# Performance work log

Measured on AMD Instinct MI355X. Metric: run time of the kernel, lower is better.

## Reference

```python
import jax, jax.numpy as jnp
import numpy as np

B, N, K = 16, 1024, 20
IN_DIM, OUT_DIM = 3, 40
LIN_DIM, HID = 1024, 512
EPS = 1e-5
NEG = 0.2  # leaky relu slope (act_kwargs negative_slope=0.2)


def setup_inputs() -> dict:
    key = jax.random.key(0)
    ks = jax.random.split(key, 9)
    def w(k, shp, scale=0.05):
        return jax.random.normal(k, shp, jnp.float32) * scale
    return {
        "pos": jax.random.normal(ks[0], (B, N, IN_DIM), jnp.float32),
        "k": K,
        "W1": w(ks[1], (2 * IN_DIM, 64)), "b1": jnp.zeros((64,), jnp.float32),
        "W2": w(ks[2], (128, 64)),        "b2": jnp.zeros((64,), jnp.float32),
        "W3": w(ks[3], (128, 128)),       "b3": jnp.zeros((128,), jnp.float32),
        "W4": w(ks[4], (256, 256)),       "b4": jnp.zeros((256,), jnp.float32),
        "Wl": w(ks[5], (512, LIN_DIM)),   "bl": jnp.zeros((LIN_DIM,), jnp.float32),
        "gl": jnp.ones((LIN_DIM,), jnp.float32), "betal": jnp.zeros((LIN_DIM,), jnp.float32),
        "Wm1": w(ks[6], (LIN_DIM, HID)),  "bm1": jnp.zeros((HID,), jnp.float32),
        "gm1": jnp.ones((HID,), jnp.float32), "betam1": jnp.zeros((HID,), jnp.float32),
        "Wm2": w(ks[7], (HID, OUT_DIM)),  "bm2": jnp.zeros((OUT_DIM,), jnp.float32),
    }


def _bn(x, g, b):
    # training-mode batch norm over axis 0 (biased variance, eps=1e-5)
    m = jnp.mean(x, axis=0)
    v = jnp.var(x, axis=0)
    return g * (x - m) * jax.lax.rsqrt(v + EPS) + b


def _leaky(x):
    return jnp.where(x > 0, x, NEG * x)


def _edge_conv(x, W, b, k):
    # x: [B,N,d]. Dynamic kNN on current features, edge feat [x_i, x_j - x_i],
    # single Linear (PyG MLP plain_last), max over k neighbors (self included).
    def per_cloud(xc):  # [N,d]
        n, d = xc.shape
        sq = jnp.sum(xc * xc, axis=1)
        dist = sq[:, None] + sq[None, :] - 2.0 * (xc @ xc.T)  # [N,N]
        _, idx = jax.lax.top_k(-dist, k)                       # [N,k] nearest (incl self)
        xj = xc[idx]                                           # [N,k,d]
        xi = xc[:, None, :]
        e = jnp.concatenate([jnp.broadcast_to(xi, (n, k, d)), xj - xi], axis=-1)
        h = e @ W + b                                          # [N,k,out]
        return jnp.max(h, axis=1)                              # [N,out]
    return jax.vmap(per_cloud)(x)


def reference(pos, k, W1, b1, W2, b2, W3, b3, W4, b4,
              Wl, bl, gl, betal, Wm1, bm1, gm1, betam1, Wm2, bm2):
    x1 = _edge_conv(pos, W1, b1, k)   # [B,N,64]
    x2 = _edge_conv(x1, W2, b2, k)    # [B,N,64]
    x3 = _edge_conv(x2, W3, b3, k)    # [B,N,128]
    x4 = _edge_conv(x3, W4, b4, k)    # [B,N,256]
    cat = jnp.concatenate([x1, x2, x3, x4], axis=-1)  # [B,N,512]
    Bn, Nn, C = cat.shape
    flat = cat.reshape(Bn * Nn, C)
    lin = _leaky(_bn(flat @ Wl + bl, gl, betal))      # [B*N,1024]
    pooled = jnp.max(lin.reshape(Bn, Nn, -1), axis=1) # global max pool -> [B,1024]
    h = _leaky(_bn(pooled @ Wm1 + bm1, gm1, betam1))  # [B,512] (dropout omitted)
    return h @ Wm2 + bm2                              # [B,40]
```

## Files before the change

kernel.cpp:

```cpp
#include <hip/hip_runtime.h>
#include <float.h>

#define NB 16
#define NP 1024
#define NROW (NB*NP)

__global__ void k_init(float* colsum, float* colsq, float* pmax, float* pmin) {
    int i = blockIdx.x * 256 + threadIdx.x;
    if (i < 1024) { colsum[i] = 0.f; colsq[i] = 0.f; }
    pmax[i] = -FLT_MAX;
    pmin[i] =  FLT_MAX;
}

__global__ void k_prep(const float* __restrict__ W, const float* __restrict__ b,
                       float* __restrict__ wc, float* __restrict__ b2, int d, int dout) {
    int n2 = 2 * dout;
    int i = blockIdx.x * 256 + threadIdx.x;
    if (i < d * n2) {
        int kk = i / n2, c = i % n2;
        wc[i] = (c < dout) ? (W[kk * dout + c] - W[(kk + d) * dout + c])
                           : W[(kk + d) * dout + (c - dout)];
    }
    if (i < n2) b2[i] = (i < dout) ? b[i] : 0.f;
}

__global__ void k_sqnorm(const float* __restrict__ x, int stride, int D, float* __restrict__ sq) {
    int row = blockIdx.x * 4 + (threadIdx.x >> 6);
    int lane = threadIdx.x & 63;
    const float* xr = x + (size_t)row * stride;
    float s = 0.f;
    for (int kk = lane; kk < D; kk += 64) { float v = xr[kk]; s += v * v; }
    for (int o = 32; o; o >>= 1) s += __shfl_down(s, o);
    if (lane == 0) sq[row] = s;
}

__device__ inline unsigned ford(float f) {
    unsigned u = __float_as_uint(f);
    return (u & 0x80000000u) ? ~u : (u | 0x80000000u);
}

#define FMA16(a, bv) do { \
    acc[0].x += (a).x*(bv).x; acc[0].y += (a).x*(bv).y; acc[0].z += (a).x*(bv).z; acc[0].w += (a).x*(bv).w; \
    acc[1].x += (a).y*(bv).x; acc[1].y += (a).y*(bv).y; acc[1].z += (a).y*(bv).z; acc[1].w += (a).y*(bv).w; \
    acc[2].x += (a).z*(bv).x; acc[2].y += (a).z*(bv).y; acc[2].z += (a).z*(bv).z; acc[2].w += (a).z*(bv).w; \
    acc[3].x += (a).w*(bv).x; acc[3].y += (a).w*(bv).y; acc[3].z += (a).w*(bv).z; acc[3].w += (a).w*(bv).w; \
} while (0)

template<int D>
__global__ __launch_bounds__(256) void k_dist(const float* __restrict__ x, int stride,
                                              const float* __restrict__ sq,
                                              float* __restrict__ dist, int pass) {
    constexpr int KC = (D > 64) ? 64 : D;
    __shared__ __align__(16) float At[KC * 68];
    __shared__ __align__(16) float Bt[KC * 64];
    const int tid = threadIdx.x;
    const int tx = tid & 15, ty = tid >> 4;
    const int j0 = blockIdx.x * 64;
    const int r0 = blockIdx.y * 64;
    const int c8 = blockIdx.z;
    const int bb = pass * 8 + c8;

    float4 acc[4] = {};
    for (int k0 = 0; k0 < D; k0 += KC) {
        __syncthreads();
        if constexpr (KC % 4 == 0) {
            constexpr int K4 = KC / 4;
            for (int e = tid; e < 64 * K4; e += 256) {
                int rr = e / K4, kq = e % K4;
                float4 v = *(const float4*)(x + (size_t)(bb * NP + r0 + rr) * stride + k0 + kq * 4);
                At[(4 * kq + 0) * 68 + rr] = v.x;
                At[(4 * kq + 1) * 68 + rr] = v.y;
                At[(4 * kq + 2) * 68 + rr] = v.z;
                At[(4 * kq + 3) * 68 + rr] = v.w;
            }
            for (int e = tid; e < 64 * K4; e += 256) {
                int jj = e / K4, kq = e % K4;
                float4 v = *(const float4*)(x + (size_t)(bb * NP + j0 + jj) * stride + k0 + kq * 4);
                Bt[(4 * kq + 0) * 64 + jj] = v.x;
                Bt[(4 * kq + 1) * 64 + jj] = v.y;
                Bt[(4 * kq + 2) * 64 + jj] = v.z;
                Bt[(4 * kq + 3) * 64 + jj] = v.w;
            }
        } else {
            for (int e = tid; e < 64 * KC; e += 256) {
                int rr = e / KC, kk = e % KC;
                At[kk * 68 + rr] = x[(size_t)(bb * NP + r0 + rr) * stride + k0 + kk];
            }
            for (int e = tid; e < 64 * KC; e += 256) {
                int jj = e / KC, kk = e % KC;
                Bt[kk * 64 + jj] = x[(size_t)(bb * NP + j0 + jj) * stride + k0 + kk];
            }
        }
        __syncthreads();
#pragma unroll 8
        for (int kk = 0; kk < KC; kk++) {
            float4 a = *(const float4*)&At[kk * 68 + ty * 4];
            float4 bv = *(const float4*)&Bt[kk * 64 + tx * 4];
            FMA16(a, bv);
        }
    }
    float4 sqv = *(const float4*)(sq + bb * NP + j0 + tx * 4);
#pragma unroll
    for (int ri = 0; ri < 4; ri++) {
        float4 o;
        o.x = sqv.x - 2.f * acc[ri].x;
        o.y = sqv.y - 2.f * acc[ri].y;
        o.z = sqv.z - 2.f * acc[ri].z;
        o.w = sqv.w - 2.f * acc[ri].w;
        *(float4*)(dist + (size_t)(c8 * NP + r0 + ty * 4 + ri) * NP + j0 + tx * 4) = o;
    }
}

__global__ __launch_bounds__(256) void k_select(const float* __restrict__ dist,
                                                int* __restrict__ idxout, int pass) {
    const int w = threadIdx.x >> 6, lane = threadIdx.x & 63;
    const int rowlocal = blockIdx.x * 4 + w;
    const size_t base = (size_t)rowlocal * NP;
    const int growrow = pass * 8 * NP + rowlocal;

    unsigned long long pk[16];
    const float4* dp = (const float4*)(dist + base + lane * 16);
#pragma unroll
    for (int q = 0; q < 4; q++) {
        float4 v = dp[q];
        int jb = lane * 16 + q * 4;
        pk[q * 4 + 0] = ((unsigned long long)ford(v.x) << 32) | (unsigned)(jb + 0);
        pk[q * 4 + 1] = ((unsigned long long)ford(v.y) << 32) | (unsigned)(jb + 1);
        pk[q * 4 + 2] = ((unsigned long long)ford(v.z) << 32) | (unsigned)(jb + 2);
        pk[q * 4 + 3] = ((unsigned long long)ford(v.w) << 32) | (unsigned)(jb + 3);
    }
    unsigned msk = 0;
#pragma unroll 1
    for (int it = 0; it < 20; it++) {
        unsigned long long m = 0xFFFFFFFFFFFFFFFFULL;
#pragma unroll
        for (int t = 0; t < 16; t++) {
            unsigned long long v = (msk & (1u << t)) ? 0xFFFFFFFFFFFFFFFFULL : pk[t];
            m = (v < m) ? v : m;
        }
#pragma unroll
        for (int o = 32; o; o >>= 1) {
            unsigned long long v = __shfl_xor(m, o);
            m = (v < m) ? v : m;
        }
        unsigned wj = (unsigned)(m & 0xFFFFFFFFu);
        if (lane == (int)(wj >> 4)) msk |= 1u << (wj & 15u);
        if (lane == 0) idxout[(size_t)growrow * 20 + it] = (int)wj;
    }
}

template<int D, int DOUT>
__global__ __launch_bounds__(256) void k_gemm_pq(const float* __restrict__ x, int stride,
                                                 const float* __restrict__ wc, const float* __restrict__ b2,
                                                 float* __restrict__ pq) {
    constexpr int N2 = 2 * DOUT;
    constexpr int KC = (D > 64) ? 64 : D;
    __shared__ __align__(16) float At[KC * 68];
    __shared__ __align__(16) float Bs[KC * 64];
    const int tid = threadIdx.x;
    const int tx = tid & 15, ty = tid >> 4;
    const int r0 = blockIdx.x * 64;
    const int c0 = blockIdx.y * 64;

    float4 acc[4] = {};
    for (int k0 = 0; k0 < D; k0 += KC) {
        __syncthreads();
        if constexpr (KC % 4 == 0) {
            constexpr int K4 = KC / 4;
            for (int e = tid; e < 64 * K4; e += 256) {
                int rr = e / K4, kq = e % K4;
                float4 v = *(const float4*)(x + (size_t)(r0 + rr) * stride + k0 + kq * 4);
                At[(4 * kq + 0) * 68 + rr] = v.x;
                At[(4 * kq + 1) * 68 + rr] = v.y;
                At[(4 * kq + 2) * 68 + rr] = v.z;
                At[(4 * kq + 3) * 68 + rr] = v.w;
            }
        } else {
            for (int e = tid; e < 64 * KC; e += 256) {
                int rr = e / KC, kk = e % KC;
                At[kk * 68 + rr] = x[(size_t)(r0 + rr) * stride + k0 + kk];
            }
        }
        for (int e = tid; e < KC * 16; e += 256) {
            int kk = e / 16, cq = e % 16;
            *(float4*)&Bs[kk * 64 + cq * 4] = *(const float4*)(wc + (size_t)(k0 + kk) * N2 + c0 + cq * 4);
        }
        __syncthreads();
#pragma unroll 8
        for (int kk = 0; kk < KC; kk++) {
            float4 a = *(const float4*)&At[kk * 68 + ty * 4];
            float4 bv = *(const float4*)&Bs[kk * 64 + tx * 4];
            FMA16(a, bv);
        }
    }
    float4 bias = *(const float4*)(b2 + c0 + tx * 4);
#pragma unroll
    for (int ri = 0; ri < 4; ri++) {
        float4 o;
        o.x = acc[ri].x + bias.x; o.y = acc[ri].y + bias.y;
        o.z = acc[ri].z + bias.z; o.w = acc[ri].w + bias.w;
        *(float4*)(pq + (size_t)(r0 + ty * 4 + ri) * N2 + c0 + tx * 4) = o;
    }
}

__global__ void k_gather(const float* __restrict__ pq, const int* __restrict__ idx,
                         float* __restrict__ cat_, int log2dout, int off) {
    int gid = blockIdx.x * 256 + threadIdx.x;
    int dout = 1 << log2dout;
    int row = gid >> log2dout;
    int c = gid & (dout - 1);
    int b = row >> 10;
    int s2 = dout * 2;
    const float* qb = pq + (size_t)(b << 10) * s2 + dout + c;
    const int* ip = idx + (size_t)row * 20;
    float m = -FLT_MAX;
#pragma unroll
    for (int t = 0; t < 20; t++) {
        int j = ip[t];
        m = fmaxf(m, qb[(size_t)j * s2]);
    }
    cat_[(size_t)row * 512 + off + c] = pq[(size_t)row * s2 + c] + m;
}

__global__ __launch_bounds__(256) void k_fused_lin(const float* __restrict__ cat_, const float* __restrict__ Wl,
                                                   const float* __restrict__ bl,
                                                   float* colsum, float* colsq, float* pmax, float* pmin) {
    __shared__ __align__(16) float At[32 * 68];
    __shared__ __align__(16) float Bs[32 * 64];
    __shared__ float red[16 * 64];
    const int tid = threadIdx.x;
    const int tx = tid & 15, ty = tid >> 4;
    const int ct = blockIdx.x, b = blockIdx.y, rs = blockIdx.z;
    const int c0 = ct * 64;

    float4 blv = *(const float4*)(bl + c0 + tx * 4);
    float4 s = {0, 0, 0, 0}, ss = {0, 0, 0, 0};
    float4 mx = {-FLT_MAX, -FLT_MAX, -FLT_MAX, -FLT_MAX};
    float4 mn = {FLT_MAX, FLT_MAX, FLT_MAX, FLT_MAX};

    for (int rt = 0; rt < 4; rt++) {
        int r0 = b * 1024 + rs * 256 + rt * 64;
        float4 acc[4] = {};
        for (int kt = 0; kt < 16; kt++) {
            __syncthreads();
            for (int e = tid; e < 512; e += 256) {
                int rr = e >> 3, kq = e & 7;
                float4 v = *(const float4*)(cat_ + (size_t)(r0 + rr) * 512 + kt * 32 + kq * 4);
                At[(4 * kq + 0) * 68 + rr] = v.x;
                At[(4 * kq + 1) * 68 + rr] = v.y;
                At[(4 * kq + 2) * 68 + rr] = v.z;
                At[(4 * kq + 3) * 68 + rr] = v.w;
            }
            for (int e = tid; e < 512; e += 256) {
                int kk = e >> 4, cq = e & 15;
                *(float4*)&Bs[kk * 64 + cq * 4] = *(const float4*)(Wl + (size_t)(kt * 32 + kk) * 1024 + c0 + cq * 4);
            }
            __syncthreads();
#pragma unroll 8
            for (int kk = 0; kk < 32; kk++) {
                float4 a = *(const float4*)&At[kk * 68 + ty * 4];
                float4 bv = *(const float4*)&Bs[kk * 64 + tx * 4];
                FMA16(a, bv);
            }
        }
#pragma unroll
        for (int ri = 0; ri < 4; ri++) {
            float yx = acc[ri].x + blv.x, yy = acc[ri].y + blv.y;
            float yz = acc[ri].z + blv.z, yw = acc[ri].w + blv.w;
            s.x += yx; ss.x += yx * yx; mx.x = fmaxf(mx.x, yx); mn.x = fminf(mn.x, yx);
            s.y += yy; ss.y += yy * yy; mx.y = fmaxf(mx.y, yy); mn.y = fminf(mn.y, yy);
            s.z += yz; ss.z += yz * yz; mx.z = fmaxf(mx.z, yz); mn.z = fminf(mn.z, yz);
            s.w += yw; ss.w += yw * yw; mx.w = fmaxf(mx.w, yw); mn.w = fminf(mn.w, yw);
        }
    }

    float rsum = 0.f, rss = 0.f, rmx = -FLT_MAX, rmn = FLT_MAX;
    __syncthreads(); *(float4*)&red[ty * 64 + tx * 4] = s;  __syncthreads();
    if (tid < 64) for (int t = 0; t < 16; t++) rsum += red[t * 64 + tid];
    __syncthreads(); *(float4*)&red[ty * 64 + tx * 4] = ss; __syncthreads();
    if (tid < 64) for (int t = 0; t < 16; t++) rss += red[t * 64 + tid];
    __syncthreads(); *(float4*)&red[ty * 64 + tx * 4] = mx; __syncthreads();
    if (tid < 64) for (int t = 0; t < 16; t++) rmx = fmaxf(rmx, red[t * 64 + tid]);
    __syncthreads(); *(float4*)&red[ty * 64 + tx * 4] = mn; __syncthreads();
    if (tid < 64) for (int t = 0; t < 16; t++) rmn = fminf(rmn, red[t * 64 + tid]);

    if (tid < 64) {
        int c = c0 + tid;
        atomicAdd(&colsum[c], rsum);
        atomicAdd(&colsq[c], rss);
        pmax[(size_t)(rs * 16 + b) * 1024 + c] = rmx;
        pmin[(size_t)(rs * 16 + b) * 1024 + c] = rmn;
    }
}

__global__ void k_bnpool(const float* colsum, const float* colsq,
                         const float* pmax, const float* pmin,
                         const float* __restrict__ gl, const float* __restrict__ betal,
                         float* __restrict__ pooled) {
    int gid = blockIdx.x * 256 + threadIdx.x;
    int c = gid & 1023, b = gid >> 10;
    float mean = colsum[c] * (1.f / 16384.f);
    float var = colsq[c] * (1.f / 16384.f) - mean * mean;
    float a = gl[c] * rsqrtf(var + 1e-5f);
    float d = betal[c] - mean * a;
    float vmx = -FLT_MAX, vmn = FLT_MAX;
#pragma unroll
    for (int rs = 0; rs < 4; rs++) {
        vmx = fmaxf(vmx, pmax[(size_t)(rs * 16 + b) * 1024 + c]);
        vmn = fminf(vmn, pmin[(size_t)(rs * 16 + b) * 1024 + c]);
    }
    float v = a * ((a >= 0.f) ? vmx : vmn) + d;
    pooled[gid] = v > 0.f ? v : 0.2f * v;
}

__global__ __launch_bounds__(256) void k_mlp1(const float* __restrict__ pooled, const float* __restrict__ Wm1,
                                              const float* __restrict__ bm1, const float* __restrict__ gm1,
                                              const float* __restrict__ betam1, float* __restrict__ hbuf) {
    int tid = threadIdx.x;
    int r = tid >> 4, cl = tid & 15;
    int c = blockIdx.x * 16 + cl;
    float z = bm1[c];
    const float* pr = pooled + (size_t)r * 1024;
    for (int kk = 0; kk < 1024; kk++) z += pr[kk] * Wm1[(size_t)kk * 512 + c];
    __shared__ float zb[16 * 16];
    zb[r * 16 + cl] = z;
    __syncthreads();
    float sm = 0.f, sq = 0.f;
#pragma unroll
    for (int rr = 0; rr < 16; rr++) { float v = zb[rr * 16 + cl]; sm += v; sq += v * v; }
    float mean = sm * (1.f / 16.f);
    float var = sq * (1.f / 16.f) - mean * mean;
    float h = gm1[c] * (z - mean) * rsqrtf(var + 1e-5f) + betam1[c];
    hbuf[(size_t)r * 512 + c] = h > 0.f ? h : 0.2f * h;
}

__global__ void k_mlp2(const float* __restrict__ hbuf, const float* __restrict__ Wm2,
                       const float* __restrict__ bm2, float* __restrict__ out) {
    int gid = blockIdx.x * 256 + threadIdx.x;
    if (gid >= 640) return;
    int r = gid / 40, c = gid % 40;
    float o = bm2[c];
    const float* hr = hbuf + (size_t)r * 512;
    for (int kk = 0; kk < 512; kk++) o += hr[kk] * Wm2[(size_t)kk * 40 + c];
    out[gid] = o;
}

extern "C" void kernel_launch(void* const* d_in, const int* in_sizes, int n_in,
                              void* d_out, int out_size, void* d_ws, size_t ws_size,
                              hipStream_t stream) {
    const float* pos = (const float*)d_in[0];
    const float* W1 = (const float*)d_in[2];
    const float* b1 = (const float*)d_in[3];
    const float* W2 = (const float*)d_in[4];
    const float* b2 = (const float*)d_in[5];
    const float* W3 = (const float*)d_in[6];
    const float* b3 = (const float*)d_in[7];
    const float* W4 = (const float*)d_in[8];
    const float* b4 = (const float*)d_in[9];
    const float* Wl = (const float*)d_in[10];
    const float* bl = (const float*)d_in[11];
    const float* gl = (const float*)d_in[12];
    const float* betal = (const float*)d_in[13];
    const float* Wm1 = (const float*)d_in[14];
    const float* bm1 = (const float*)d_in[15];
    const float* gm1 = (const float*)d_in[16];
    const float* betam1 = (const float*)d_in[17];
    const float* Wm2 = (const float*)d_in[18];
    const float* bm2 = (const float*)d_in[19];
    float* out = (float*)d_out;

    float* ws = (float*)d_ws;
    float* cat_ = ws;
    float* pq = cat_ + (size_t)NROW * 512;
    int* idx = (int*)(pq + (size_t)NROW * 512);
    float* sqb = (float*)(idx + NROW * 20);
    float* wc1 = sqb + NROW;
    float* wc2 = wc1 + 3 * 128;
    float* wc3 = wc2 + 64 * 128;
    float* wc4 = wc3 + 64 * 256;
    float* bb1 = wc4 + 128 * 512;
    float* bb2 = bb1 + 128;
    float* bb3 = bb2 + 128;
    float* bb4 = bb3 + 256;
    float* colsum = bb4 + 512;
    float* colsq = colsum + 1024;
    float* pmax = colsq + 1024;
    float* pmin = pmax + 4 * NROW;
    float* pooled = pmin + 4 * NROW;
    float* hbuf = pooled + NROW;
    size_t need = (size_t)((hbuf + 16 * 512) - ws) * sizeof(float);
    if (ws_size < need) return;

    float* dist = pq;

    k_init<<<256, 256, 0, stream>>>(colsum, colsq, pmax, pmin);
    k_prep<<<256, 256, 0, stream>>>(W1, b1, wc1, bb1, 3, 64);
    k_prep<<<256, 256, 0, stream>>>(W2, b2, wc2, bb2, 64, 64);
    k_prep<<<256, 256, 0, stream>>>(W3, b3, wc3, bb3, 64, 128);
    k_prep<<<256, 256, 0, stream>>>(W4, b4, wc4, bb4, 128, 256);

    k_sqnorm<<<4096, 256, 0, stream>>>(pos, 3, 3, sqb);
    for (int p = 0; p < 2; p++) {
        k_dist<3><<<dim3(16, 16, 8), 256, 0, stream>>>(pos, 3, sqb, dist, p);
        k_select<<<2048, 256, 0, stream>>>(dist, idx, p);
    }
    k_gemm_pq<3, 64><<<dim3(256, 2), 256, 0, stream>>>(pos, 3, wc1, bb1, pq);
    k_gather<<<4096, 256, 0, stream>>>(pq, idx, cat_, 6, 0);
    k_sqnorm<<<4096, 256, 0, stream>>>(cat_, 512, 64, sqb);
    for (int p = 0; p < 2; p++) {
        k_dist<64><<<dim3(16, 16, 8), 256, 0, stream>>>(cat_, 512, sqb, dist, p);
        k_select<<<2048, 256, 0, stream>>>(dist, idx, p);
    }
    k_gemm_pq<64, 64><<<dim3(256, 2), 256, 0, stream>>>(cat_, 512, wc2, bb2, pq);
    k_gather<<<4096, 256, 0, stream>>>(pq, idx, cat_, 6, 64);
    k_sqnorm<<<4096, 256, 0, stream>>>(cat_ + 64, 512, 64, sqb);
    for (int p = 0; p < 2; p++) {
        k_dist<64><<<dim3(16, 16, 8), 256, 0, stream>>>(cat_ + 64, 512, sqb, dist, p);
        k_select<<<2048, 256, 0, stream>>>(dist, idx, p);
    }
    k_gemm_pq<64, 128><<<dim3(256, 4), 256, 0, stream>>>(cat_ + 64, 512, wc3, bb3, pq);
    k_gather<<<8192, 256, 0, stream>>>(pq, idx, cat_, 7, 128);
    k_sqnorm<<<4096, 256, 0, stream>>>(cat_ + 128, 512, 128, sqb);
    for (int p = 0; p < 2; p++) {
        k_dist<128><<<dim3(16, 16, 8), 256, 0, stream>>>(cat_ + 128, 512, sqb, dist, p);
        k_select<<<2048, 256, 0, stream>>>(dist, idx, p);
    }
    k_gemm_pq<128, 256><<<dim3(256, 8), 256, 0, stream>>>(cat_ + 128, 512, wc4, bb4, pq);
    k_gather<<<16384, 256, 0, stream>>>(pq, idx, cat_, 8, 256);

    k_fused_lin<<<dim3(16, 16, 4), 256, 0, stream>>>(cat_, Wl, bl, colsum, colsq, pmax, pmin);
    k_bnpool<<<64, 256, 0, stream>>>(colsum, colsq, pmax, pmin, gl, betal, pooled);
    k_mlp1<<<32, 256, 0, stream>>>(pooled, Wm1, bm1, gm1, betam1, hbuf);
    k_mlp2<<<3, 256, 0, stream>>>(hbuf, Wm2, bm2, out);
}
```

Baseline: 1.040 ms.

## Enlarge dist and final-linear GEMM tiles to 128x128 with 8x8 per-thread blocking

The pairwise-distance kernel and the fused final-linear kernel move from 64x64 tiles with 4x4 register blocks to 128x128 tiles with 8x8 register blocks. This raises arithmetic intensity and cuts shared-memory traffic per FMA. The final-linear kernel now reduces per-128-row slice, so the max/min partials grow from 4 to 8 slices; these buffers are aliased into the pq scratch and initialized just before use. The cost is higher register pressure and fewer blocks, which may lower occupancy.

```diff
diff --git a/kernel.cpp b/kernel.cpp
--- a/kernel.cpp
+++ b/kernel.cpp
@@ -39,6 +39,11 @@
     return (u & 0x80000000u) ? ~u : (u | 0x80000000u);
 }
 
+#define FMA8(c0_, c1_, s_, b0_, b1_) do { \
+    (c0_).x += (s_)*(b0_).x; (c0_).y += (s_)*(b0_).y; (c0_).z += (s_)*(b0_).z; (c0_).w += (s_)*(b0_).w; \
+    (c1_).x += (s_)*(b1_).x; (c1_).y += (s_)*(b1_).y; (c1_).z += (s_)*(b1_).z; (c1_).w += (s_)*(b1_).w; \
+} while (0)
+
 #define FMA16(a, bv) do { \
     acc[0].x += (a).x*(bv).x; acc[0].y += (a).x*(bv).y; acc[0].z += (a).x*(bv).z; acc[0].w += (a).x*(bv).w; \
     acc[1].x += (a).y*(bv).x; acc[1].y += (a).y*(bv).y; acc[1].z += (a).y*(bv).z; acc[1].w += (a).y*(bv).w; \
@@ -50,64 +55,75 @@
 __global__ __launch_bounds__(256) void k_dist(const float* __restrict__ x, int stride,
                                               const float* __restrict__ sq,
                                               float* __restrict__ dist, int pass) {
-    constexpr int KC = (D > 64) ? 64 : D;
-    __shared__ __align__(16) float At[KC * 68];
-    __shared__ __align__(16) float Bt[KC * 64];
+    constexpr int KC = (D < 32) ? D : 32;
+    __shared__ __align__(16) float At[KC * 132];
+    __shared__ __align__(16) float Bt[KC * 132];
     const int tid = threadIdx.x;
     const int tx = tid & 15, ty = tid >> 4;
-    const int j0 = blockIdx.x * 64;
-    const int r0 = blockIdx.y * 64;
-    const int c8 = blockIdx.z;
-    const int bb = pass * 8 + c8;
-
-    float4 acc[4] = {};
+    const int j0 = blockIdx.x * 128;
+    const int r0 = blockIdx.y * 128;
+    const int bb = pass * 8 + blockIdx.z;
+
+    float4 acc0[8] = {}, acc1[8] = {};
     for (int k0 = 0; k0 < D; k0 += KC) {
         __syncthreads();
         if constexpr (KC % 4 == 0) {
             constexpr int K4 = KC / 4;
-            for (int e = tid; e < 64 * K4; e += 256) {
+            for (int e = tid; e < 128 * K4; e += 256) {
                 int rr = e / K4, kq = e % K4;
                 float4 v = *(const float4*)(x + (size_t)(bb * NP + r0 + rr) * stride + k0 + kq * 4);
-                At[(4 * kq + 0) * 68 + rr] = v.x;
-                At[(4 * kq + 1) * 68 + rr] = v.y;
-                At[(4 * kq + 2) * 68 + rr] = v.z;
-                At[(4 * kq + 3) * 68 + rr] = v.w;
-            }
-            for (int e = tid; e < 64 * K4; e += 256) {
+                At[(4 * kq + 0) * 132 + rr] = v.x;
+                At[(4 * kq + 1) * 132 + rr] = v.y;
+                At[(4 * kq + 2) * 132 + rr] = v.z;
+                At[(4 * kq + 3) * 132 + rr] = v.w;
+            }
+            for (int e = tid; e < 128 * K4; e += 256) {
                 int jj = e / K4, kq = e % K4;
                 float4 v = *(const float4*)(x + (size_t)(bb * NP + j0 + jj) * stride + k0 + kq * 4);
-                Bt[(4 * kq + 0) * 64 + jj] = v.x;
-                Bt[(4 * kq + 1) * 64 + jj] = v.y;
-                Bt[(4 * kq + 2) * 64 + jj] = v.z;
-                Bt[(4 * kq + 3) * 64 + jj] = v.w;
+                Bt[(4 * kq + 0) * 132 + jj] = v.x;
+                Bt[(4 * kq + 1) * 132 + jj] = v.y;
+                Bt[(4 * kq + 2) * 132 + jj] = v.z;
+                Bt[(4 * kq + 3) * 132 + jj] = v.w;
             }
         } else {
-            for (int e = tid; e < 64 * KC; e += 256) {
+            for (int e = tid; e < 128 * KC; e += 256) {
                 int rr = e / KC, kk = e % KC;
-                At[kk * 68 + rr] = x[(size_t)(bb * NP + r0 + rr) * stride + k0 + kk];
-            }
-            for (int e = tid; e < 64 * KC; e += 256) {
+                At[kk * 132 + rr] = x[(size_t)(bb * NP + r0 + rr) * stride + k0 + kk];
+            }
+            for (int e = tid; e < 128 * KC; e += 256) {
                 int jj = e / KC, kk = e % KC;
-                Bt[kk * 64 + jj] = x[(size_t)(bb * NP + j0 + jj) * stride + k0 + kk];
-            }
-        }
-        __syncthreads();
-#pragma unroll 8
+                Bt[kk * 132 + jj] = x[(size_t)(bb * NP + j0 + jj) * stride + k0 + kk];
+            }
+        }
+        __syncthreads();
+#pragma unroll 4
         for (int kk = 0; kk < KC; kk++) {
-            float4 a = *(const float4*)&At[kk * 68 + ty * 4];
-            float4 bv = *(const float4*)&Bt[kk * 64 + tx * 4];
-            FMA16(a, bv);
-        }
-    }
-    float4 sqv = *(const float4*)(sq + bb * NP + j0 + tx * 4);
-#pragma unroll
-    for (int ri = 0; ri < 4; ri++) {
-        float4 o;
-        o.x = sqv.x - 2.f * acc[ri].x;
-        o.y = sqv.y - 2.f * acc[ri].y;
-        o.z = sqv.z - 2.f * acc[ri].z;
-        o.w = sqv.w - 2.f * acc[ri].w;
-        *(float4*)(dist + (size_t)(c8 * NP + r0 + ty * 4 + ri) * NP + j0 + tx * 4) = o;
+            float4 a0 = *(const float4*)&At[kk * 132 + ty * 8];
+            float4 a1 = *(const float4*)&At[kk * 132 + ty * 8 + 4];
+            float4 b0 = *(const float4*)&Bt[kk * 132 + tx * 8];
+            float4 b1 = *(const float4*)&Bt[kk * 132 + tx * 8 + 4];
+            FMA8(acc0[0], acc1[0], a0.x, b0, b1);
+            FMA8(acc0[1], acc1[1], a0.y, b0, b1);
+            FMA8(acc0[2], acc1[2], a0.z, b0, b1);
+            FMA8(acc0[3], acc1[3], a0.w, b0, b1);
+            FMA8(acc0[4], acc1[4], a1.x, b0, b1);
+            FMA8(acc0[5], acc1[5], a1.y, b0, b1);
+            FMA8(acc0[6], acc1[6], a1.z, b0, b1);
+            FMA8(acc0[7], acc1[7], a1.w, b0, b1);
+        }
+    }
+    float4 sq0 = *(const float4*)(sq + bb * NP + j0 + tx * 8);
+    float4 sq1 = *(const float4*)(sq + bb * NP + j0 + tx * 8 + 4);
+#pragma unroll
+    for (int ri = 0; ri < 8; ri++) {
+        float* dp = dist + (size_t)(blockIdx.z * NP + r0 + ty * 8 + ri) * NP + j0 + tx * 8;
+        float4 o0, o1;
+        o0.x = sq0.x - 2.f * acc0[ri].x; o0.y = sq0.y - 2.f * acc0[ri].y;
+        o0.z = sq0.z - 2.f * acc0[ri].z; o0.w = sq0.w - 2.f * acc0[ri].w;
+        o1.x = sq1.x - 2.f * acc1[ri].x; o1.y = sq1.y - 2.f * acc1[ri].y;
+        o1.z = sq1.z - 2.f * acc1[ri].z; o1.w = sq1.w - 2.f * acc1[ri].w;
+        *(float4*)dp = o0;
+        *(float4*)(dp + 4) = o1;
     }
 }
 
@@ -225,71 +241,95 @@
 __global__ __launch_bounds__(256) void k_fused_lin(const float* __restrict__ cat_, const float* __restrict__ Wl,
                                                    const float* __restrict__ bl,
                                                    float* colsum, float* colsq, float* pmax, float* pmin) {
-    __shared__ __align__(16) float At[32 * 68];
-    __shared__ __align__(16) float Bs[32 * 64];
-    __shared__ float red[16 * 64];
+    __shared__ __align__(16) float At[32 * 132];
+    __shared__ __align__(16) float Bs[32 * 132];
+    __shared__ float red[16 * 128];
     const int tid = threadIdx.x;
     const int tx = tid & 15, ty = tid >> 4;
-    const int ct = blockIdx.x, b = blockIdx.y, rs = blockIdx.z;
-    const int c0 = ct * 64;
-
-    float4 blv = *(const float4*)(bl + c0 + tx * 4);
-    float4 s = {0, 0, 0, 0}, ss = {0, 0, 0, 0};
-    float4 mx = {-FLT_MAX, -FLT_MAX, -FLT_MAX, -FLT_MAX};
-    float4 mn = {FLT_MAX, FLT_MAX, FLT_MAX, FLT_MAX};
-
-    for (int rt = 0; rt < 4; rt++) {
-        int r0 = b * 1024 + rs * 256 + rt * 64;
-        float4 acc[4] = {};
-        for (int kt = 0; kt < 16; kt++) {
-            __syncthreads();
-            for (int e = tid; e < 512; e += 256) {
-                int rr = e >> 3, kq = e & 7;
-                float4 v = *(const float4*)(cat_ + (size_t)(r0 + rr) * 512 + kt * 32 + kq * 4);
-                At[(4 * kq + 0) * 68 + rr] = v.x;
-                At[(4 * kq + 1) * 68 + rr] = v.y;
-                At[(4 * kq + 2) * 68 + rr] = v.z;
-                At[(4 * kq + 3) * 68 + rr] = v.w;
-            }
-            for (int e = tid; e < 512; e += 256) {
-                int kk = e >> 4, cq = e & 15;
-                *(float4*)&Bs[kk * 64 + cq * 4] = *(const float4*)(Wl + (size_t)(kt * 32 + kk) * 1024 + c0 + cq * 4);
-            }
-            __syncthreads();
-#pragma unroll 8
-            for (int kk = 0; kk < 32; kk++) {
-                float4 a = *(const float4*)&At[kk * 68 + ty * 4];
-                float4 bv = *(const float4*)&Bs[kk * 64 + tx * 4];
-                FMA16(a, bv);
-            }
-        }
-#pragma unroll
-        for (int ri = 0; ri < 4; ri++) {
-            float yx = acc[ri].x + blv.x, yy = acc[ri].y + blv.y;
-            float yz = acc[ri].z + blv.z, yw = acc[ri].w + blv.w;
-            s.x += yx; ss.x += yx * yx; mx.x = fmaxf(mx.x, yx); mn.x = fminf(mn.x, yx);
-            s.y += yy; ss.y += yy * yy; mx.y = fmaxf(mx.y, yy); mn.y = fminf(mn.y, yy);
-            s.z += yz; ss.z += yz * yz; mx.z = fmaxf(mx.z, yz); mn.z = fminf(mn.z, yz);
-            s.w += yw; ss.w += yw * yw; mx.w = fmaxf(mx.w, yw); mn.w = fminf(mn.w, yw);
-        }
+    const int c0 = blockIdx.x * 128;
+    const int rb = blockIdx.y;
+    const int r0 = rb * 128;
+
+    float4 acc0[8] = {}, acc1[8] = {};
+    for (int kt = 0; kt < 16; kt++) {
+        __syncthreads();
+        for (int e = tid; e < 128 * 8; e += 256) {
+            int rr = e >> 3, kq = e & 7;
+            float4 v = *(const float4*)(cat_ + (size_t)(r0 + rr) * 512 + kt * 32 + kq * 4);
+            At[(4 * kq + 0) * 132 + rr] = v.x;
+            At[(4 * kq + 1) * 132 + rr] = v.y;
+            At[(4 * kq + 2) * 132 + rr] = v.z;
+            At[(4 * kq + 3) * 132 + rr] = v.w;
+        }
+        for (int e = tid; e < 32 * 32; e += 256) {
+            int kk = e >> 5, cq = e & 31;
+            *(float4*)&Bs[kk * 132 + cq * 4] = *(const float4*)(Wl + (size_t)(kt * 32 + kk) * 1024 + c0 + cq * 4);
+        }
+        __syncthreads();
+#pragma unroll 4
+        for (int kk = 0; kk < 32; kk++) {
+            float4 a0 = *(const float4*)&At[kk * 132 + ty * 8];
+            float4 a1 = *(const float4*)&At[kk * 132 + ty * 8 + 4];
+            float4 b0 = *(const float4*)&Bs[kk * 132 + tx * 8];
+            float4 b1 = *(const float4*)&Bs[kk * 132 + tx * 8 + 4];
+            FMA8(acc0[0], acc1[0], a0.x, b0, b1);
+            FMA8(acc0[1], acc1[1], a0.y, b0, b1);
+            FMA8(acc0[2], acc1[2], a0.z, b0, b1);
+            FMA8(acc0[3], acc1[3], a0.w, b0, b1);
+            FMA8(acc0[4], acc1[4], a1.x, b0, b1);
+            FMA8(acc0[5], acc1[5], a1.y, b0, b1);
+            FMA8(acc0[6], acc1[6], a1.z, b0, b1);
+            FMA8(acc0[7], acc1[7], a1.w, b0, b1);
+        }
+    }
+
+    float4 bl0 = *(const float4*)(bl + c0 + tx * 8);
+    float4 bl1 = *(const float4*)(bl + c0 + tx * 8 + 4);
+    float4 s0 = {0,0,0,0}, s1 = {0,0,0,0}, ss0 = {0,0,0,0}, ss1 = {0,0,0,0};
+    float4 mx0 = {-FLT_MAX,-FLT_MAX,-FLT_MAX,-FLT_MAX}, mx1 = mx0;
+    float4 mn0 = {FLT_MAX,FLT_MAX,FLT_MAX,FLT_MAX}, mn1 = mn0;
+#pragma unroll
+    for (int ri = 0; ri < 8; ri++) {
+        float4 y0, y1;
+        y0.x = acc0[ri].x + bl0.x; y0.y = acc0[ri].y + bl0.y;
+        y0.z = acc0[ri].z + bl0.z; y0.w = acc0[ri].w + bl0.w;
+        y1.x = acc1[ri].x + bl1.x; y1.y = acc1[ri].y + bl1.y;
+        y1.z = acc1[ri].z + bl1.z; y1.w = acc1[ri].w + bl1.w;
+        s0.x += y0.x; ss0.x += y0.x*y0.x; mx0.x = fmaxf(mx0.x, y0.x); mn0.x = fminf(mn0.x, y0.x);
+        s0.y += y0.y; ss0.y += y0.y*y0.y; mx0.y = fmaxf(mx0.y, y0.y); mn0.y = fminf(mn0.y, y0.y);
+        s0.z += y0.z; ss0.z += y0.z*y0.z; mx0.z = fmaxf(mx0.z, y0.z); mn0.z = fminf(mn0.z, y0.z);
+        s0.w += y0.w; ss0.w += y0.w*y0.w; mx0.w = fmaxf(mx0.w, y0.w); mn0.w = fminf(mn0.w, y0.w);
+        s1.x += y1.x; ss1.x += y1.x*y1.x; mx1.x = fmaxf(mx1.x, y1.x); mn1.x = fminf(mn1.x, y1.x);
+        s1.y += y1.y; ss1.y += y1.y*y1.y; mx1.y = fmaxf(mx1.y, y1.y); mn1.y = fminf(mn1.y, y1.y);
+        s1.z += y1.z; ss1.z += y1.z*y1.z; mx1.z = fmaxf(mx1.z, y1.z); mn1.z = fminf(mn1.z, y1.z);
+        s1.w += y1.w; ss1.w += y1.w*y1.w; mx1.w = fmaxf(mx1.w, y1.w); mn1.w = fminf(mn1.w, y1.w);
     }
 
     float rsum = 0.f, rss = 0.f, rmx = -FLT_MAX, rmn = FLT_MAX;
-    __syncthreads(); *(float4*)&red[ty * 64 + tx * 4] = s;  __syncthreads();
-    if (tid < 64) for (int t = 0; t < 16; t++) rsum += red[t * 64 + tid];
-    __syncthreads(); *(float4*)&red[ty * 64 + tx * 4] = ss; __syncthreads();
-    if (tid < 64) for (int t = 0; t < 16; t++) rss += red[t * 64 + tid];
-    __syncthreads(); *(float4*)&red[ty * 64 + tx * 4] = mx; __syncthreads();
-    if (tid < 64) for (int t = 0; t < 16; t++) rmx = fmaxf(rmx, red[t * 64 + tid]);
-    __syncthreads(); *(float4*)&red[ty * 64 + tx * 4] = mn; __syncthreads();
-    if (tid < 64) for (int t = 0; t < 16; t++) rmn = fminf(rmn, red[t * 64 + tid]);
-
-    if (tid < 64) {
+    __syncthreads();
+    *(float4*)&red[ty * 128 + tx * 8] = s0; *(float4*)&red[ty * 128 + tx * 8 + 4] = s1;
+    __syncthreads();
+    if (tid < 128) for (int t = 0; t < 16; t++) rsum += red[t * 128 + tid];
+    __syncthreads();
+    *(float4*)&red[ty * 128 + tx * 8] = ss0; *(float4*)&red[ty * 128 + tx * 8 + 4] = ss1;
+    __syncthreads();
+    if (tid < 128) for (int t = 0; t < 16; t++) rss += red[t * 128 + tid];
+    __syncthreads();
+    *(float4*)&red[ty * 128 + tx * 8] = mx0; *(float4*)&red[ty * 128 + tx * 8 + 4] = mx1;
+    __syncthreads();
+    if (tid < 128) for (int t = 0; t < 16; t++) rmx = fmaxf(rmx, red[t * 128 + tid]);
+    __syncthreads();
+    *(float4*)&red[ty * 128 + tx * 8] = mn0; *(float4*)&red[ty * 128 + tx * 8 + 4] = mn1;
+    __syncthreads();
+    if (tid < 128) for (int t = 0; t < 16; t++) rmn = fminf(rmn, red[t * 128 + tid]);
+
+    if (tid < 128) {
         int c = c0 + tid;
+        int b = rb >> 3, slice = rb & 7;
         atomicAdd(&colsum[c], rsum);
         atomicAdd(&colsq[c], rss);
-        pmax[(size_t)(rs * 16 + b) * 1024 + c] = rmx;
-        pmin[(size_t)(rs * 16 + b) * 1024 + c] = rmn;
+        pmax[(size_t)(slice * 16 + b) * 1024 + c] = rmx;
+        pmin[(size_t)(slice * 16 + b) * 1024 + c] = rmn;
     }
 }
 
@@ -305,7 +345,7 @@
     float d = betal[c] - mean * a;
     float vmx = -FLT_MAX, vmn = FLT_MAX;
 #pragma unroll
-    for (int rs = 0; rs < 4; rs++) {
+    for (int rs = 0; rs < 8; rs++) {
         vmx = fmaxf(vmx, pmax[(size_t)(rs * 16 + b) * 1024 + c]);
         vmn = fminf(vmn, pmin[(size_t)(rs * 16 + b) * 1024 + c]);
     }
@@ -384,16 +424,15 @@
     float* bb4 = bb3 + 256;
     float* colsum = bb4 + 512;
     float* colsq = colsum + 1024;
-    float* pmax = colsq + 1024;
-    float* pmin = pmax + 4 * NROW;
-    float* pooled = pmin + 4 * NROW;
+    float* pooled = colsq + 1024;
     float* hbuf = pooled + NROW;
     size_t need = (size_t)((hbuf + 16 * 512) - ws) * sizeof(float);
     if (ws_size < need) return;
 
     float* dist = pq;
-
-    k_init<<<256, 256, 0, stream>>>(colsum, colsq, pmax, pmin);
+    float* pmax = pq;
+    float* pmin = pq + 8 * 16 * 1024;
+
     k_prep<<<256, 256, 0, stream>>>(W1, b1, wc1, bb1, 3, 64);
     k_prep<<<256, 256, 0, stream>>>(W2, b2, wc2, bb2, 64, 64);
     k_prep<<<256, 256, 0, stream>>>(W3, b3, wc3, bb3, 64, 128);
@@ -401,34 +440,35 @@
 
     k_sqnorm<<<4096, 256, 0, stream>>>(pos, 3, 3, sqb);
     for (int p = 0; p < 2; p++) {
-        k_dist<3><<<dim3(16, 16, 8), 256, 0, stream>>>(pos, 3, sqb, dist, p);
+        k_dist<3><<<dim3(8, 8, 8), 256, 0, stream>>>(pos, 3, sqb, dist, p);
         k_select<<<2048, 256, 0, stream>>>(dist, idx, p);
     }
     k_gemm_pq<3, 64><<<dim3(256, 2), 256, 0, stream>>>(pos, 3, wc1, bb1, pq);
     k_gather<<<4096, 256, 0, stream>>>(pq, idx, cat_, 6, 0);
     k_sqnorm<<<4096, 256, 0, stream>>>(cat_, 512, 64, sqb);
     for (int p = 0; p < 2; p++) {
-        k_dist<64><<<dim3(16, 16, 8), 256, 0, stream>>>(cat_, 512, sqb, dist, p);
+        k_dist<64><<<dim3(8, 8, 8), 256, 0, stream>>>(cat_, 512, sqb, dist, p);
         k_select<<<2048, 256, 0, stream>>>(dist, idx, p);
     }
     k_gemm_pq<64, 64><<<dim3(256, 2), 256, 0, stream>>>(cat_, 512, wc2, bb2, pq);
     k_gather<<<4096, 256, 0, stream>>>(pq, idx, cat_, 6, 64);
     k_sqnorm<<<4096, 256, 0, stream>>>(cat_ + 64, 512, 64, sqb);
     for (int p = 0; p < 2; p++) {
-        k_dist<64><<<dim3(16, 16, 8), 256, 0, stream>>>(cat_ + 64, 512, sqb, dist, p);
+        k_dist<64><<<dim3(8, 8, 8), 256, 0, stream>>>(cat_ + 64, 512, sqb, dist, p);
         k_select<<<2048, 256, 0, stream>>>(dist, idx, p);
     }
     k_gemm_pq<64, 128><<<dim3(256, 4), 256, 0, stream>>>(cat_ + 64, 512, wc3, bb3, pq);
     k_gather<<<8192, 256, 0, stream>>>(pq, idx, cat_, 7, 128);
     k_sqnorm<<<4096, 256, 0, stream>>>(cat_ + 128, 512, 128, sqb);
     for (int p = 0; p < 2; p++) {
-        k_dist<128><<<dim3(16, 16, 8), 256, 0, stream>>>(cat_ + 128, 512, sqb, dist, p);
+        k_dist<128><<<dim3(8, 8, 8), 256, 0, stream>>>(cat_ + 128, 512, sqb, dist, p);
         k_select<<<2048, 256, 0, stream>>>(dist, idx, p);
     }
     k_gemm_pq<128, 256><<<dim3(256, 8), 256, 0, stream>>>(cat_ + 128, 512, wc4, bb4, pq);
     k_gather<<<16384, 256, 0, stream>>>(pq, idx, cat_, 8, 256);
 
-    k_fused_lin<<<dim3(16, 16, 4), 256, 0, stream>>>(cat_, Wl, bl, colsum, colsq, pmax, pmin);
+    k_init<<<512, 256, 0, stream>>>(colsum, colsq, pmax, pmin);
+    k_fused_lin<<<dim3(8, 128), 256, 0, stream>>>(cat_, Wl, bl, colsum, colsq, pmax, pmin);
     k_bnpool<<<64, 256, 0, stream>>>(colsum, colsq, pmax, pmin, gl, betal, pooled);
     k_mlp1<<<32, 256, 0, stream>>>(pooled, Wm1, bm1, gm1, betam1, hbuf);
     k_mlp2<<<3, 256, 0, stream>>>(hbuf, Wm2, bm2, out);
```

Measured after the change: 967.5 us. 1.08x faster.
